# Kernel tuning notes

Hardware: AMD Instinct MI355X
Metric: run time of the kernel (lower is better)

## Reference

```python
import jax, jax.numpy as jnp
import numpy as np

B, N, E = 128, 2048, 32768   # events, nodes per history graph, temporal edges per graph
C, TC, H = 4, 4, 2           # channels, time_channels, heads (hardcoded in source)
DH = C // H
L = 2                        # num_layers


def setup_inputs() -> dict:
    key = jax.random.key(0)
    ks = jax.random.split(key, 16)
    return {
        "x": jax.random.normal(ks[0], (B, N, C), jnp.float32),
        "edge_index": jax.random.randint(ks[1], (B, 2, E), 0, N),
        "edge_time": jax.random.uniform(ks[2], (B, E), jnp.float32),
        "timestamp": jax.random.uniform(ks[3], (B,), jnp.float32),
        "src_index": jax.random.randint(ks[4], (B,), 0, N),
        "dst_index": jax.random.randint(ks[5], (B,), 0, N),
        "time_w": jax.random.normal(ks[6], (TC,), jnp.float32),
        "time_b": jax.random.normal(ks[7], (TC,), jnp.float32),
        "Wq": jax.random.normal(ks[8], (L, C, C), jnp.float32) / np.sqrt(C).astype(np.float32),
        "Wk": jax.random.normal(ks[9], (L, C + TC, C), jnp.float32) / np.sqrt(C + TC).astype(np.float32),
        "Wv": jax.random.normal(ks[10], (L, C + TC, C), jnp.float32) / np.sqrt(C + TC).astype(np.float32),
        "Wo": jax.random.normal(ks[11], (L, C, C), jnp.float32) / np.sqrt(C).astype(np.float32),
        "bo": jnp.zeros((L, C), jnp.float32),
        "W_lin": jax.random.normal(ks[12], (2 * C + TC, 2), jnp.float32) / np.sqrt(2 * C + TC).astype(np.float32),
        "b_lin": jnp.zeros((2,), jnp.float32),
    }


def _time_enc(t, w, b):
    # TimeEncoder: cos(t * w + b)  (Bochner-style functional time encoding)
    return jnp.cos(t[..., None] * w + b)


def _encode(x, src, dst, phi, Wq, Wk, Wv, Wo, bo):
    # seg id per edge: (batch, dst node) -> flat segment for segment softmax
    seg = (jnp.arange(B, dtype=dst.dtype)[:, None] * N + dst).reshape(-1)  # [B*E]
    h = x
    for l in range(L):
        h_src = jnp.take_along_axis(h, src[:, :, None], axis=1)            # [B,E,C] gather source feats
        msg = jnp.concatenate([h_src, phi], axis=-1)                       # [B,E,C+TC]
        q = (h @ Wq[l]).reshape(B, N, C)                                   # [B,N,C]
        k = (msg @ Wk[l]).reshape(B, E, H, DH)
        v = (msg @ Wv[l]).reshape(B, E, H, DH)
        q_e = jnp.take_along_axis(q, dst[:, :, None], axis=1).reshape(B, E, H, DH)
        logits = (q_e * k).sum(-1) / np.float32(np.sqrt(DH))               # [B,E,H]
        lf = logits.reshape(B * E, H)
        m = jax.ops.segment_max(lf, seg, num_segments=B * N)               # stable softmax max
        p = jnp.exp(lf - m[seg])
        s = jax.ops.segment_sum(p, seg, num_segments=B * N)
        agg = jax.ops.segment_sum(p[:, :, None] * v.reshape(B * E, H, DH), seg, num_segments=B * N)
        attn = (agg / jnp.where(s == 0, 1.0, s)[:, :, None]).reshape(B, N, C)
        h = jax.nn.relu(h + attn @ Wo[l] + bo[l])                          # residual + out-proj + relu
    return h


def reference(x, edge_index, edge_time, timestamp, src_index, dst_index,
              time_w, time_b, Wq, Wk, Wv, Wo, bo, W_lin, b_lin):
    src, dst = edge_index[:, 0, :], edge_index[:, 1, :]
    dt = timestamp[:, None] - edge_time                                    # [B,E] time deltas vs query time
    phi = _time_enc(dt, time_w, time_b)                                    # [B,E,TC]
    h = _encode(x, src, dst, phi, Wq, Wk, Wv, Wo, bo)                      # [B,N,C]
    bidx = jnp.arange(B)
    src_x = h[bidx, src_index]                                             # [B,C]
    dst_x = h[bidx, dst_index]                                             # [B,C]
    time_x = _time_enc(timestamp, time_w, time_b)                          # [B,TC]
    feats = jnp.concatenate([src_x, dst_x, time_x], axis=-1)               # [B,12]
    return feats @ W_lin + b_lin                                           # [B,2]
```

## Files before the change

### kernel.cpp

```cpp
#include <hip/hip_runtime.h>
#include <hip/hip_fp16.h>

namespace {

constexpr int B = 128, N = 2048, E = 32768;
constexpr int LOG2N = 11, LOG2E = 15;
constexpr int DMAX = 128;

constexpr size_t OFF_H0  = 0;
constexpr size_t OFF_H1  = 4u * 1024 * 1024;
constexpr size_t OFF_ELL = 8u * 1024 * 1024;
constexpr size_t OFF_NR  = 136u * 1024 * 1024;
constexpr size_t OFF_INV = 138u * 1024 * 1024;

__global__ __launch_bounds__(1024) void sort_kernel(const int* __restrict__ edge_index,
                                                    const float* __restrict__ edge_time,
                                                    const float* __restrict__ timestamp,
                                                    unsigned* __restrict__ ell,
                                                    unsigned* __restrict__ nr_out,
                                                    int* __restrict__ inv_out) {
  __shared__ int      cnt[N];
  __shared__ int      rbase[N];
  __shared__ int      partial[1024];
  __shared__ unsigned nrp[N];
  __shared__ int      dhist[64];
  __shared__ unsigned rec[E];
  int b = blockIdx.x, t = threadIdx.x;
  const int* src_arr = edge_index + ((size_t)(2 * b) << LOG2E);
  const int* dst_arr = src_arr + E;
  const float* et    = edge_time + ((size_t)b << LOG2E);
  float ts = timestamp[b];

  cnt[t] = 0; cnt[t + 1024] = 0;
  if (t < 64) dhist[t] = 0;
  __syncthreads();

  for (int e = t; e < E; e += 1024) atomicAdd(&cnt[dst_arr[e]], 1);
  __syncthreads();

  int i0 = 2 * t, i1 = 2 * t + 1;
  int l0 = cnt[i0], l1 = cnt[i1], sum = l0 + l1;
  partial[t] = sum;
  __syncthreads();
  for (int d = 1; d < 1024; d <<= 1) {
    int v = (t >= d) ? partial[t - d] : 0;
    __syncthreads();
    partial[t] += v;
    __syncthreads();
  }
  int run = partial[t] - sum;
  rbase[i0] = run;      rbase[i1] = run + l0;
  cnt[i0]   = run;      cnt[i1]   = run + l0;
  __syncthreads();

  for (int e = t; e < E; e += 1024) {
    int dst = dst_arr[e], src = src_arr[e];
    float dt = ts - et[e];
    unsigned hd = (unsigned)__half_as_ushort(__float2half(dt));
    int pos = atomicAdd(&cnt[dst], 1);
    rec[pos] = (unsigned)src | (hd << 16);
  }
  __syncthreads();

  for (int n = t; n < N; n += 1024) {
    int deg = cnt[n] - rbase[n];
    atomicAdd(&dhist[min(deg, 63)], 1);
  }
  __syncthreads();
  if (t == 0) {
    int acc = 0;
    for (int k = 0; k < 64; k++) { int c = dhist[k]; dhist[k] = acc; acc += c; }
  }
  __syncthreads();

  for (int n = t; n < N; n += 1024) {
    int deg = cnt[n] - rbase[n];
    int r = atomicAdd(&dhist[min(deg, 63)], 1);
    nrp[r] = (unsigned)n | ((unsigned)deg << 16);
    inv_out[((size_t)b << LOG2N) + n] = r;
  }
  __syncthreads();

  nr_out[((size_t)b << LOG2N) + t] = nrp[t];
  nr_out[((size_t)b << LOG2N) + t + 1024] = nrp[t + 1024];

  size_t ebase = (size_t)b * DMAX * N;
  for (int r = t; r < N; r += 1024) {
    unsigned pk = nrp[r];
    int n = pk & 0xFFFF;
    int deg = min((int)(pk >> 16), DMAX);
    int base = rbase[n];
    for (int j = 0; j < deg; j++)
      ell[ebase + ((size_t)j << LOG2N) + r] = rec[base + j];
  }
}

__global__ __launch_bounds__(1024) void layer_kernel(const float4* __restrict__ h_in,
                                                     int in_ranked,
                                                     float4* __restrict__ h_out,
                                                     const unsigned* __restrict__ nr_g,
                                                     const unsigned* __restrict__ ell,
                                                     const float* __restrict__ tw,
                                                     const float* __restrict__ tb,
                                                     const float* __restrict__ Wq,
                                                     const float* __restrict__ Wk,
                                                     const float* __restrict__ Wv,
                                                     const float* __restrict__ Wo,
                                                     const float* __restrict__ bo) {
  __shared__ float4   lh[N];
  __shared__ unsigned lnr[N];
  int blk = blockIdx.x, b = blk >> 1, rh = blk & 1, t = threadIdx.x;

  unsigned pk0 = nr_g[((size_t)b << LOG2N) + t];
  unsigned pk1 = nr_g[((size_t)b << LOG2N) + t + 1024];
  lnr[t] = pk0; lnr[t + 1024] = pk1;
  const float4* hb = h_in + ((size_t)b << LOG2N);
  float4 s0v = hb[t], s1v = hb[t + 1024];
  if (in_ranked) {
    lh[pk0 & 0xFFFF] = s0v;
    lh[pk1 & 0xFFFF] = s1v;
  } else {
    lh[t] = s0v;
    lh[t + 1024] = s1v;
  }

  float twf[4], tbf[4], bof[4], wq[16], wof[16], wk[32], wv[32];
#pragma unroll
  for (int j = 0; j < 4; j++) { twf[j] = tw[j]; tbf[j] = tb[j]; bof[j] = bo[j]; }
#pragma unroll
  for (int j = 0; j < 16; j++) { wq[j] = Wq[j]; wof[j] = Wo[j]; }
#pragma unroll
  for (int j = 0; j < 32; j++) { wk[j] = Wk[j]; wv[j] = Wv[j]; }
  __syncthreads();

  int r = (rh << 10) + t;
  unsigned pk = lnr[r];
  int n = pk & 0xFFFF;
  int deg = min((int)(pk >> 16), DMAX);
  float4 hn = lh[n];
  float q0 = hn.x * wq[0] + hn.y * wq[4] + hn.z * wq[8]  + hn.w * wq[12];
  float q1 = hn.x * wq[1] + hn.y * wq[5] + hn.z * wq[9]  + hn.w * wq[13];
  float q2 = hn.x * wq[2] + hn.y * wq[6] + hn.z * wq[10] + hn.w * wq[14];
  float q3 = hn.x * wq[3] + hn.y * wq[7] + hn.z * wq[11] + hn.w * wq[15];
  const float RS2 = 0.70710678118654752f;
  float u0[8], u1[8];
#pragma unroll
  for (int j = 0; j < 8; j++) {
    u0[j] = RS2 * (q0 * wk[j * 4 + 0] + q1 * wk[j * 4 + 1]);
    u1[j] = RS2 * (q2 * wk[j * 4 + 2] + q3 * wk[j * 4 + 3]);
  }

  float m0 = -INFINITY, m1 = -INFINITY;
  float s0 = 0.f, s1 = 0.f, a00 = 0.f, a01 = 0.f, a10 = 0.f, a11 = 0.f;
  const unsigned* eb = ell + (size_t)b * DMAX * N + r;

  unsigned rc = (deg > 0) ? eb[0] : 0u;
  for (int j = 0; j < deg; ++j) {
    unsigned rc_next = (j + 1 < deg) ? eb[(size_t)(j + 1) << LOG2N] : 0u;
    int src = rc & 0xFFFF;
    float dt = __half2float(__ushort_as_half((unsigned short)(rc >> 16)));
    float4 hs = lh[src];
    float p0c = __cosf(dt * twf[0] + tbf[0]);
    float p1c = __cosf(dt * twf[1] + tbf[1]);
    float p2c = __cosf(dt * twf[2] + tbf[2]);
    float p3c = __cosf(dt * twf[3] + tbf[3]);
    float l0 = u0[0] * hs.x + u0[1] * hs.y + u0[2] * hs.z + u0[3] * hs.w
             + u0[4] * p0c + u0[5] * p1c + u0[6] * p2c + u0[7] * p3c;
    float l1 = u1[0] * hs.x + u1[1] * hs.y + u1[2] * hs.z + u1[3] * hs.w
             + u1[4] * p0c + u1[5] * p1c + u1[6] * p2c + u1[7] * p3c;
    float v0 = wv[0] * hs.x + wv[4] * hs.y + wv[8]  * hs.z + wv[12] * hs.w
             + wv[16] * p0c + wv[20] * p1c + wv[24] * p2c + wv[28] * p3c;
    float v1 = wv[1] * hs.x + wv[5] * hs.y + wv[9]  * hs.z + wv[13] * hs.w
             + wv[17] * p0c + wv[21] * p1c + wv[25] * p2c + wv[29] * p3c;
    float v2 = wv[2] * hs.x + wv[6] * hs.y + wv[10] * hs.z + wv[14] * hs.w
             + wv[18] * p0c + wv[22] * p1c + wv[26] * p2c + wv[30] * p3c;
    float v3 = wv[3] * hs.x + wv[7] * hs.y + wv[11] * hs.z + wv[15] * hs.w
             + wv[19] * p0c + wv[23] * p1c + wv[27] * p2c + wv[31] * p3c;
    float nm0 = fmaxf(m0, l0);
    float sc0 = __expf(m0 - nm0);
    float p0  = __expf(l0 - nm0);
    s0 = s0 * sc0 + p0; a00 = a00 * sc0 + p0 * v0; a01 = a01 * sc0 + p0 * v1; m0 = nm0;
    float nm1 = fmaxf(m1, l1);
    float sc1 = __expf(m1 - nm1);
    float p1  = __expf(l1 - nm1);
    s1 = s1 * sc1 + p1; a10 = a10 * sc1 + p1 * v2; a11 = a11 * sc1 + p1 * v3; m1 = nm1;
    rc = rc_next;
  }
  float d0 = (s0 == 0.f) ? 1.f : s0;
  float d1 = (s1 == 0.f) ? 1.f : s1;
  float at0 = a00 / d0, at1 = a01 / d0, at2 = a10 / d1, at3 = a11 / d1;
  float o0 = bof[0] + at0 * wof[0] + at1 * wof[4] + at2 * wof[8]  + at3 * wof[12];
  float o1 = bof[1] + at0 * wof[1] + at1 * wof[5] + at2 * wof[9]  + at3 * wof[13];
  float o2 = bof[2] + at0 * wof[2] + at1 * wof[6] + at2 * wof[10] + at3 * wof[14];
  float o3 = bof[3] + at0 * wof[3] + at1 * wof[7] + at2 * wof[11] + at3 * wof[15];
  h_out[((size_t)b << LOG2N) + r] =
      make_float4(fmaxf(hn.x + o0, 0.f), fmaxf(hn.y + o1, 0.f),
                  fmaxf(hn.z + o2, 0.f), fmaxf(hn.w + o3, 0.f));
}

__global__ void final_kernel(const float4* __restrict__ h,
                             const int* __restrict__ inv,
                             const int* __restrict__ src_index, const int* __restrict__ dst_index,
                             const float* __restrict__ timestamp,
                             const float* __restrict__ tw,
                             const float* __restrict__ tb,
                             const float* __restrict__ W_lin,
                             const float* __restrict__ b_lin,
                             float* __restrict__ out) {
  int b = threadIdx.x;
  if (b >= B) return;
  int rs = inv[((size_t)b << LOG2N) + src_index[b]];
  int rd = inv[((size_t)b << LOG2N) + dst_index[b]];
  float4 sx = h[((size_t)b << LOG2N) + rs];
  float4 dx = h[((size_t)b << LOG2N) + rd];
  float ts = timestamp[b];
  float f[12];
  f[0] = sx.x; f[1] = sx.y; f[2] = sx.z; f[3] = sx.w;
  f[4] = dx.x; f[5] = dx.y; f[6] = dx.z; f[7] = dx.w;
#pragma unroll
  for (int j = 0; j < 4; j++) f[8 + j] = __cosf(ts * tw[j] + tb[j]);
#pragma unroll
  for (int c = 0; c < 2; c++) {
    float o = b_lin[c];
#pragma unroll
    for (int j = 0; j < 12; j++) o += f[j] * W_lin[j * 2 + c];
    out[b * 2 + c] = o;
  }
}

}

extern "C" void kernel_launch(void* const* d_in, const int* in_sizes, int n_in,
                              void* d_out, int out_size, void* d_ws, size_t ws_size,
                              hipStream_t stream) {
  (void)in_sizes; (void)n_in; (void)out_size; (void)ws_size;
  const float* x         = (const float*)d_in[0];
  const int*   edge_idx  = (const int*)d_in[1];
  const float* edge_time = (const float*)d_in[2];
  const float* timestamp = (const float*)d_in[3];
  const int*   src_index = (const int*)d_in[4];
  const int*   dst_index = (const int*)d_in[5];
  const float* time_w    = (const float*)d_in[6];
  const float* time_b    = (const float*)d_in[7];
  const float* Wq        = (const float*)d_in[8];
  const float* Wk        = (const float*)d_in[9];
  const float* Wv        = (const float*)d_in[10];
  const float* Wo        = (const float*)d_in[11];
  const float* bo        = (const float*)d_in[12];
  const float* W_lin     = (const float*)d_in[13];
  const float* b_lin     = (const float*)d_in[14];

  char* ws = (char*)d_ws;
  float4*   h0  = (float4*)(ws + OFF_H0);
  float4*   h1  = (float4*)(ws + OFF_H1);
  unsigned* ell = (unsigned*)(ws + OFF_ELL);
  unsigned* nr  = (unsigned*)(ws + OFF_NR);
  int*      inv = (int*)(ws + OFF_INV);

  sort_kernel<<<B, 1024, 0, stream>>>(edge_idx, edge_time, timestamp, ell, nr, inv);

  layer_kernel<<<2 * B, 1024, 0, stream>>>((const float4*)x, 0, h1, nr, ell,
                                           time_w, time_b,
                                           Wq + 0 * 16, Wk + 0 * 32, Wv + 0 * 32,
                                           Wo + 0 * 16, bo + 0 * 4);
  layer_kernel<<<2 * B, 1024, 0, stream>>>(h1, 1, h0, nr, ell,
                                           time_w, time_b,
                                           Wq + 1 * 16, Wk + 1 * 32, Wv + 1 * 32,
                                           Wo + 1 * 16, bo + 1 * 4);

  final_kernel<<<1, 128, 0, stream>>>(h0, inv, src_index, dst_index, timestamp,
                                      time_w, time_b, W_lin, b_lin, (float*)d_out);
}
```

Before: 202.4 us.

## Split edge sort across two blocks per graph by destination half

The sort kernel now launches two blocks per graph. Each block handles only edges whose destination falls in its half of the nodes, so shared memory per block shrinks and twice as many CUs take part. Degree ranking and the ELL layout become local to each half, and the layer kernel indexes per-half ELL slabs to match. DMAX drops to 64 and the per-half record buffer has a fixed capacity. That assumes degrees and per-half edge counts stay within those bounds, and each block now reads the full edge list twice while filtering.

After: 201.5 us. No clear change (-0.4%).

```diff
diff --git a/kernel.cpp b/kernel.cpp
--- a/kernel.cpp
+++ b/kernel.cpp
@@ -5,13 +5,14 @@
 
 constexpr int B = 128, N = 2048, E = 32768;
 constexpr int LOG2N = 11, LOG2E = 15;
-constexpr int DMAX = 128;
+constexpr int DMAX = 64;
+constexpr int RECCAP = 17408;
 
 constexpr size_t OFF_H0  = 0;
 constexpr size_t OFF_H1  = 4u * 1024 * 1024;
 constexpr size_t OFF_ELL = 8u * 1024 * 1024;
-constexpr size_t OFF_NR  = 136u * 1024 * 1024;
-constexpr size_t OFF_INV = 138u * 1024 * 1024;
+constexpr size_t OFF_NR  = 72u * 1024 * 1024;
+constexpr size_t OFF_INV = 74u * 1024 * 1024;
 
 __global__ __launch_bounds__(1024) void sort_kernel(const int* __restrict__ edge_index,
                                                     const float* __restrict__ edge_time,
@@ -19,28 +20,31 @@
                                                     unsigned* __restrict__ ell,
                                                     unsigned* __restrict__ nr_out,
                                                     int* __restrict__ inv_out) {
-  __shared__ int      cnt[N];
-  __shared__ int      rbase[N];
+  __shared__ int      cnt[1024];
+  __shared__ int      rbase[1024];
   __shared__ int      partial[1024];
-  __shared__ unsigned nrp[N];
+  __shared__ unsigned nrp[1024];
   __shared__ int      dhist[64];
-  __shared__ unsigned rec[E];
-  int b = blockIdx.x, t = threadIdx.x;
+  __shared__ unsigned rec[RECCAP];
+  int blk = blockIdx.x, b = blk >> 1, hr = blk & 1, t = threadIdx.x;
+  int lo = hr << 10;
   const int* src_arr = edge_index + ((size_t)(2 * b) << LOG2E);
   const int* dst_arr = src_arr + E;
   const float* et    = edge_time + ((size_t)b << LOG2E);
   float ts = timestamp[b];
 
-  cnt[t] = 0; cnt[t + 1024] = 0;
+  cnt[t] = 0;
   if (t < 64) dhist[t] = 0;
   __syncthreads();
 
-  for (int e = t; e < E; e += 1024) atomicAdd(&cnt[dst_arr[e]], 1);
-  __syncthreads();
-
-  int i0 = 2 * t, i1 = 2 * t + 1;
-  int l0 = cnt[i0], l1 = cnt[i1], sum = l0 + l1;
-  partial[t] = sum;
+  for (int e = t; e < E; e += 1024) {
+    int d = dst_arr[e];
+    if ((d >> 10) == hr) atomicAdd(&cnt[d & 1023], 1);
+  }
+  __syncthreads();
+
+  int c = cnt[t];
+  partial[t] = c;
   __syncthreads();
   for (int d = 1; d < 1024; d <<= 1) {
     int v = (t >= d) ? partial[t - d] : 0;
@@ -48,51 +52,42 @@
     partial[t] += v;
     __syncthreads();
   }
-  int run = partial[t] - sum;
-  rbase[i0] = run;      rbase[i1] = run + l0;
-  cnt[i0]   = run;      cnt[i1]   = run + l0;
-  __syncthreads();
-
-  for (int e = t; e < E; e += 1024) {
-    int dst = dst_arr[e], src = src_arr[e];
-    float dt = ts - et[e];
-    unsigned hd = (unsigned)__half_as_ushort(__float2half(dt));
-    int pos = atomicAdd(&cnt[dst], 1);
-    rec[pos] = (unsigned)src | (hd << 16);
-  }
-  __syncthreads();
-
-  for (int n = t; n < N; n += 1024) {
-    int deg = cnt[n] - rbase[n];
-    atomicAdd(&dhist[min(deg, 63)], 1);
-  }
+  int run = partial[t] - c;
+  rbase[t] = run;
+  cnt[t] = run;
+  int deg = c;
+  atomicAdd(&dhist[min(deg, 63)], 1);
   __syncthreads();
   if (t == 0) {
     int acc = 0;
-    for (int k = 0; k < 64; k++) { int c = dhist[k]; dhist[k] = acc; acc += c; }
-  }
-  __syncthreads();
-
-  for (int n = t; n < N; n += 1024) {
-    int deg = cnt[n] - rbase[n];
-    int r = atomicAdd(&dhist[min(deg, 63)], 1);
-    nrp[r] = (unsigned)n | ((unsigned)deg << 16);
-    inv_out[((size_t)b << LOG2N) + n] = r;
-  }
-  __syncthreads();
-
-  nr_out[((size_t)b << LOG2N) + t] = nrp[t];
-  nr_out[((size_t)b << LOG2N) + t + 1024] = nrp[t + 1024];
-
-  size_t ebase = (size_t)b * DMAX * N;
-  for (int r = t; r < N; r += 1024) {
-    unsigned pk = nrp[r];
-    int n = pk & 0xFFFF;
-    int deg = min((int)(pk >> 16), DMAX);
-    int base = rbase[n];
-    for (int j = 0; j < deg; j++)
-      ell[ebase + ((size_t)j << LOG2N) + r] = rec[base + j];
-  }
+    for (int k = 0; k < 64; k++) { int cc = dhist[k]; dhist[k] = acc; acc += cc; }
+  }
+  __syncthreads();
+  int r = atomicAdd(&dhist[min(deg, 63)], 1);
+  nrp[r] = (unsigned)(lo + t) | ((unsigned)deg << 16);
+  inv_out[((size_t)b << LOG2N) + lo + t] = lo + r;
+  __syncthreads();
+  nr_out[((size_t)b << LOG2N) + lo + t] = nrp[t];
+
+  for (int e = t; e < E; e += 1024) {
+    int d = dst_arr[e];
+    if ((d >> 10) == hr) {
+      int src = src_arr[e];
+      float dt = ts - et[e];
+      unsigned hd = (unsigned)__half_as_ushort(__float2half(dt));
+      int pos = atomicAdd(&cnt[d & 1023], 1);
+      rec[pos] = (unsigned)src | (hd << 16);
+    }
+  }
+  __syncthreads();
+
+  unsigned pk = nrp[t];
+  int nloc = (int)(pk & 1023u);
+  int dg = min((int)(pk >> 16), DMAX);
+  int base = rbase[nloc];
+  size_t ebase = (size_t)blk * DMAX * 1024;
+  for (int j = 0; j < dg; j++)
+    ell[ebase + ((size_t)j << 10) + t] = rec[base + j];
 }
 
 __global__ __launch_bounds__(1024) void layer_kernel(const float4* __restrict__ h_in,
@@ -117,8 +112,8 @@
   const float4* hb = h_in + ((size_t)b << LOG2N);
   float4 s0v = hb[t], s1v = hb[t + 1024];
   if (in_ranked) {
-    lh[pk0 & 0xFFFF] = s0v;
-    lh[pk1 & 0xFFFF] = s1v;
+    lh[pk0 & 0xFFFFu] = s0v;
+    lh[pk1 & 0xFFFFu] = s1v;
   } else {
     lh[t] = s0v;
     lh[t + 1024] = s1v;
@@ -133,9 +128,8 @@
   for (int j = 0; j < 32; j++) { wk[j] = Wk[j]; wv[j] = Wv[j]; }
   __syncthreads();
 
-  int r = (rh << 10) + t;
-  unsigned pk = lnr[r];
-  int n = pk & 0xFFFF;
+  unsigned pk = lnr[(rh << 10) + t];
+  int n = (int)(pk & 0xFFFFu);
   int deg = min((int)(pk >> 16), DMAX);
   float4 hn = lh[n];
   float q0 = hn.x * wq[0] + hn.y * wq[4] + hn.z * wq[8]  + hn.w * wq[12];
@@ -152,12 +146,12 @@
 
   float m0 = -INFINITY, m1 = -INFINITY;
   float s0 = 0.f, s1 = 0.f, a00 = 0.f, a01 = 0.f, a10 = 0.f, a11 = 0.f;
-  const unsigned* eb = ell + (size_t)b * DMAX * N + r;
+  const unsigned* eb = ell + (size_t)blk * DMAX * 1024 + t;
 
   unsigned rc = (deg > 0) ? eb[0] : 0u;
   for (int j = 0; j < deg; ++j) {
-    unsigned rc_next = (j + 1 < deg) ? eb[(size_t)(j + 1) << LOG2N] : 0u;
-    int src = rc & 0xFFFF;
+    unsigned rc_next = (j + 1 < deg) ? eb[(size_t)(j + 1) << 10] : 0u;
+    int src = (int)(rc & 0xFFFFu);
     float dt = __half2float(__ushort_as_half((unsigned short)(rc >> 16)));
     float4 hs = lh[src];
     float p0c = __cosf(dt * twf[0] + tbf[0]);
@@ -193,7 +187,7 @@
   float o1 = bof[1] + at0 * wof[1] + at1 * wof[5] + at2 * wof[9]  + at3 * wof[13];
   float o2 = bof[2] + at0 * wof[2] + at1 * wof[6] + at2 * wof[10] + at3 * wof[14];
   float o3 = bof[3] + at0 * wof[3] + at1 * wof[7] + at2 * wof[11] + at3 * wof[15];
-  h_out[((size_t)b << LOG2N) + r] =
+  h_out[((size_t)b << LOG2N) + (rh << 10) + t] =
       make_float4(fmaxf(hn.x + o0, 0.f), fmaxf(hn.y + o1, 0.f),
                   fmaxf(hn.z + o2, 0.f), fmaxf(hn.w + o3, 0.f));
 }
@@ -257,7 +251,7 @@
   unsigned* nr  = (unsigned*)(ws + OFF_NR);
   int*      inv = (int*)(ws + OFF_INV);
 
-  sort_kernel<<<B, 1024, 0, stream>>>(edge_idx, edge_time, timestamp, ell, nr, inv);
+  sort_kernel<<<2 * B, 1024, 0, stream>>>(edge_idx, edge_time, timestamp, ell, nr, inv);
 
   layer_kernel<<<2 * B, 1024, 0, stream>>>((const float4*)x, 0, h1, nr, ell,
                                            time_w, time_b,
```
